# Kernel optimization log

Hardware: AMD Instinct MI355X
Metric: run time of the kernel (lower is better)

Reference implementation:

```python
import jax, jax.numpy as jnp
import numpy as np

N = 102400      # total nodes (2048 molecules x 50 atoms)
E = 409600      # directed edges (avg degree 4)
B = 2048        # number of graphs in batch
F0 = 78         # num_features_mol
OUT = 200       # output_dim
MAXN = 64       # max_num nodes per graph (padding)


def _glorot(key, fan_in, fan_out):
    lim = jnp.sqrt(6.0 / (fan_in + fan_out)).astype(jnp.float32)
    return jax.random.uniform(key, (fan_in, fan_out), jnp.float32, -lim, lim)


def setup_inputs() -> dict:
    key = jax.random.key(0)
    ks = jax.random.split(key, 8)
    x = jax.random.normal(ks[0], (N, F0), jnp.float32)
    edge_index = jax.random.randint(ks[1], (2, E), 0, N, jnp.int32)
    # sorted contiguous graph assignment, 50 nodes per graph
    batch = jnp.repeat(jnp.arange(B, dtype=jnp.int32), N // B)
    return {
        "x": x,
        "edge_index": edge_index,
        "batch": batch,
        "max_num": MAXN,
        "W1": _glorot(ks[2], F0, F0),        "b1": jnp.zeros((F0,), jnp.float32),
        "W2": _glorot(ks[3], F0, 2 * F0),    "b2": jnp.zeros((2 * F0,), jnp.float32),
        "W3": _glorot(ks[4], 2 * F0, 4 * F0),"b3": jnp.zeros((4 * F0,), jnp.float32),
        "Wfc": _glorot(ks[5], 4 * F0, OUT),  "bfc": jnp.zeros((OUT,), jnp.float32),
    }


def _gcn_conv(h, W, b, src, dst, dinv):
    """PyG GCNConv: x' = D^{-1/2}(A+I)D^{-1/2} (x W) + b (with self-loops)."""
    h = h @ W                                  # [N, Fout]
    coef = (dinv[src] * dinv[dst])[:, None]    # [E, 1] symmetric norm
    agg = jax.ops.segment_sum(h[src] * coef, dst, num_segments=N)
    agg = agg + h * (dinv * dinv)[:, None]     # self-loop contribution (norm = 1/deg)
    return agg + b


def reference(x, edge_index, batch, max_num, W1, b1, W2, b2, W3, b3, Wfc, bfc):
    src, dst = edge_index[0], edge_index[1]
    # degree incl. self-loop, computed on destination nodes (PyG gcn_norm)
    deg = jax.ops.segment_sum(jnp.ones((E,), x.dtype), dst, num_segments=N) + 1.0
    dinv = jax.lax.rsqrt(deg)

    h = jax.nn.relu(_gcn_conv(x, W1, b1, src, dst, dinv))
    h = jax.nn.relu(_gcn_conv(h, W2, b2, src, dst, dinv))
    h = jax.nn.relu(_gcn_conv(h, W3, b3, src, dst, dinv))
    h = h @ Wfc + bfc                          # [N, OUT]

    # to_dense_batch: scatter each node into [B, max_num, OUT], truncating
    # nodes beyond max_num per graph (PyG semantics).
    counts = jax.ops.segment_sum(jnp.ones((N,), jnp.int32), batch, num_segments=B)
    starts = jnp.concatenate([jnp.zeros((1,), jnp.int32), jnp.cumsum(counts)[:-1]])
    pos = jnp.arange(N, dtype=jnp.int32) - starts[batch]   # index within graph
    valid = pos < max_num
    flat = jnp.where(valid, batch * max_num + pos, B * max_num)  # dropped -> dummy slot
    dense = jnp.zeros((B * max_num + 1, h.shape[1]), h.dtype).at[flat].set(h)
    return dense[:-1].reshape(B, max_num, h.shape[1])
```

## Files before the change

### kernel.cpp

```cpp
#include <hip/hip_runtime.h>
#include <hip/hip_bf16.h>
#include <stdint.h>

#define N_NODES 102400
#define N_EDGES 409600
#define N_GRAPHS 2048
#define MAXN 64

typedef __attribute__((ext_vector_type(8))) short short8;
typedef __attribute__((ext_vector_type(4))) float f32x4;

static __device__ __forceinline__ float bfu2f(unsigned short u) {
    union { unsigned int i; float f; } v;
    v.i = ((unsigned int)u) << 16;
    return v.f;
}
static __device__ __forceinline__ unsigned short f2bfu(float f) {
    __hip_bfloat16 h = __float2bfloat16(f);
    return *reinterpret_cast<unsigned short*>(&h);
}


__global__ void deg_kernel(const int* __restrict__ dst, int* __restrict__ deg) {
    int e = blockIdx.x * blockDim.x + threadIdx.x;
    if (e < N_EDGES) atomicAdd(&deg[dst[e]], 1);
}

__global__ void scan1_kernel(const int* __restrict__ deg, int* __restrict__ excl,
                             int* __restrict__ bsum) {
    __shared__ int sh[1024];
    int tid = threadIdx.x;
    int gid = blockIdx.x * 1024 + tid;
    int v = deg[gid];
    sh[tid] = v;
    __syncthreads();
    for (int off = 1; off < 1024; off <<= 1) {
        int t = (tid >= off) ? sh[tid - off] : 0;
        __syncthreads();
        sh[tid] += t;
        __syncthreads();
    }
    excl[gid] = sh[tid] - v;
    if (tid == 1023) bsum[blockIdx.x] = sh[tid];
}

__global__ void scan2_kernel(int* __restrict__ bsum) {
    __shared__ int sh[128];
    int tid = threadIdx.x;
    int v = (tid < 100) ? bsum[tid] : 0;
    sh[tid] = v;
    __syncthreads();
    for (int off = 1; off < 128; off <<= 1) {
        int t = (tid >= off) ? sh[tid - off] : 0;
        __syncthreads();
        sh[tid] += t;
        __syncthreads();
    }
    if (tid < 100) bsum[tid] = sh[tid] - v;
}

__global__ void scan3_kernel(const int* __restrict__ excl, const int* __restrict__ bsum,
                             const int* __restrict__ deg,
                             int* __restrict__ offs, int* __restrict__ cursor,
                             float* __restrict__ dinv) {
    int gid = blockIdx.x * blockDim.x + threadIdx.x;
    if (gid < N_NODES) {
        int o = excl[gid] + bsum[gid >> 10];
        offs[gid] = o;
        cursor[gid] = o;
        dinv[gid] = rsqrtf((float)deg[gid] + 1.0f);
    }
    if (gid == 0) offs[N_NODES] = N_EDGES;
}

__global__ void fill_kernel(const int* __restrict__ src, const int* __restrict__ dst,
                            int* __restrict__ cursor, int2* __restrict__ csr_pk,
                            const float* __restrict__ dinv) {
    int e = blockIdx.x * blockDim.x + threadIdx.x;
    if (e >= N_EDGES) return;
    int s = src[e], d = dst[e];
    int pos = atomicAdd(&cursor[d], 1);
    float w = dinv[s] * dinv[d];
    int2 pk;
    pk.x = s;
    pk.y = __float_as_int(w);
    csr_pk[pos] = pk;
}


__global__ void start_kernel(const int* __restrict__ batch, int* __restrict__ startb) {
    int i = blockIdx.x * blockDim.x + threadIdx.x;
    if (i >= N_NODES) return;
    if (i == 0 || batch[i] != batch[i - 1]) startb[batch[i]] = i;
    if (i == 0) startb[N_GRAPHS] = N_NODES;
}

__global__ void rowmap_kernel(const int* __restrict__ batch, const int* __restrict__ startb,
                              const int* __restrict__ pmax, int* __restrict__ rowmap) {
    int i = blockIdx.x * blockDim.x + threadIdx.x;
    if (i >= N_NODES) return;
    int b = batch[i];
    int mx = *pmax;
    int pos = i - startb[b];
    rowmap[i] = (pos < mx) ? (b * mx + pos) : -1;
}

__global__ void padzero_kernel(const int* __restrict__ startb, float* __restrict__ out) {
    int b = blockIdx.x;
    int count = startb[b + 1] - startb[b];
    if (count >= MAXN) return;
    int nel = (MAXN - count) * 100;
    float* base = out + ((size_t)b * MAXN + count) * 200;
    for (int i = threadIdx.x; i < nel; i += 256) {
        float2 z = {0.0f, 0.0f};
        *(float2*)(base + i * 2) = z;
    }
}


__global__ __launch_bounds__(256) void cast_x_kernel(const float* __restrict__ X,
                                                     __hip_bfloat16* __restrict__ xb) {
    int idx = blockIdx.x * blockDim.x + threadIdx.x;
    if (idx >= N_NODES * 48) return;
    int node = idx / 48;
    int c = idx - node * 48;
    int col = c * 2;
    float2 v = {0.0f, 0.0f};
    if (col < 78) v = *(const float2*)(X + (size_t)node * 78 + col);
    __hip_bfloat162 r;
    r.x = __float2bfloat16(v.x);
    r.y = __float2bfloat16(v.y);
    *(__hip_bfloat162*)(xb + (size_t)node * 96 + col) = r;
}


static __device__ __forceinline__ void prep_one(int i, const float* __restrict__ W,
                                                const float* __restrict__ b,
                                                int K, int Nc, int Kp, int Na,
                                                __hip_bfloat16* __restrict__ WT,
                                                float* __restrict__ bp) {
    int total = Na * Kp;
    if (i < total) {
        int c = i / Kp, k = i - c * Kp;
        float v = (c < Nc && k < K) ? W[k * Nc + c] : 0.0f;
        WT[i] = __float2bfloat16(v);
    }
    if (i < Na) bp[i] = (i < Nc) ? b[i] : 0.0f;
}

__global__ void prep_all_kernel(
    const float* __restrict__ W1, const float* __restrict__ b1,
    const float* __restrict__ W2, const float* __restrict__ b2,
    const float* __restrict__ W3, const float* __restrict__ b3,
    const float* __restrict__ Wf, const float* __restrict__ bf,
    __hip_bfloat16* __restrict__ WT1, float* __restrict__ b1p,
    __hip_bfloat16* __restrict__ WT2, float* __restrict__ b2p,
    __hip_bfloat16* __restrict__ WT3, float* __restrict__ b3p,
    __hip_bfloat16* __restrict__ WTF, float* __restrict__ bFp) {
    int i = blockIdx.x * blockDim.x + threadIdx.x;
    if (i < 12288) prep_one(i, W1, b1, 78, 78, 96, 128, WT1, b1p);
    else if (i < 36864) prep_one(i - 12288, W2, b2, 78, 156, 96, 256, WT2, b2p);
    else if (i < 98304) prep_one(i - 36864, W3, b3, 156, 312, 160, 384, WT3, b3p);
    else if (i < 180224) prep_one(i - 98304, Wf, bf, 312, 200, 320, 256, WTF, bFp);
}


template <int LD>
__global__ __launch_bounds__(256) void agg_bf16_v4(
    const __hip_bfloat16* __restrict__ H,
    const int* __restrict__ offs, const int2* __restrict__ csr_pk,
    const float* __restrict__ dinv,
    __hip_bfloat16* __restrict__ out) {
    constexpr int C = LD / 8;
    int idx = blockIdx.x * blockDim.x + threadIdx.x;
    if (idx >= N_NODES * C) return;
    int node = idx / C;
    int c = idx - node * C;
    const unsigned short* Hu = (const unsigned short*)H;
    size_t rowoff = (size_t)node * LD + c * 8;
    float di = dinv[node];
    float sw = di * di;
    short8 h = *(const short8*)(Hu + rowoff);
    float a[8];
#pragma unroll
    for (int i = 0; i < 8; ++i) a[i] = sw * bfu2f((unsigned short)h[i]);
    int e0 = offs[node], e1 = offs[node + 1];
    int j = e0;
    for (; j + 4 <= e1; j += 4) {
        int2 p0 = csr_pk[j], p1 = csr_pk[j + 1], p2 = csr_pk[j + 2], p3 = csr_pk[j + 3];
        float w0 = __int_as_float(p0.y), w1 = __int_as_float(p1.y);
        float w2 = __int_as_float(p2.y), w3 = __int_as_float(p3.y);
        short8 v0 = *(const short8*)(Hu + (size_t)p0.x * LD + c * 8);
        short8 v1 = *(const short8*)(Hu + (size_t)p1.x * LD + c * 8);
        short8 v2 = *(const short8*)(Hu + (size_t)p2.x * LD + c * 8);
        short8 v3 = *(const short8*)(Hu + (size_t)p3.x * LD + c * 8);
#pragma unroll
        for (int i = 0; i < 8; ++i)
            a[i] += w0 * bfu2f((unsigned short)v0[i]) + w1 * bfu2f((unsigned short)v1[i]) +
                    w2 * bfu2f((unsigned short)v2[i]) + w3 * bfu2f((unsigned short)v3[i]);
    }
    for (; j < e1; ++j) {
        int2 pk = csr_pk[j];
        float w = __int_as_float(pk.y);
        short8 v = *(const short8*)(Hu + (size_t)pk.x * LD + c * 8);
#pragma unroll
        for (int i = 0; i < 8; ++i) a[i] += w * bfu2f((unsigned short)v[i]);
    }
    short8 r;
#pragma unroll
    for (int i = 0; i < 8; ++i) r[i] = (short)f2bfu(a[i]);
    *(short8*)((unsigned short*)out + rowoff) = r;
}


template <int FOUT>
__global__ __launch_bounds__(256) void agg_gemm_kernel(
    const __hip_bfloat16* __restrict__ H,
    const int* __restrict__ offs, const int2* __restrict__ csr_pk,
    const float* __restrict__ dinv,
    const __hip_bfloat16* __restrict__ WT,
    const float* __restrict__ biasp,
    __hip_bfloat16* __restrict__ OutH) {
    constexpr int LDH = 96;
    constexpr int NB = FOUT / 32;
    constexpr int STRIDE = 208;
    __shared__ __align__(16) char aggT[128 * STRIDE];
    const int tid = threadIdx.x;
    const int r0 = blockIdx.x * 128;

    {
        const int row = tid >> 1;
        const int cb = (tid & 1) * 6;
        const int node = r0 + row;
        const unsigned short* Hu = (const unsigned short*)H;
        const unsigned short* selfp = Hu + (size_t)node * LDH + cb * 8;
        float di = dinv[node];
        float sw = di * di;
        float a[6][8];
        {
            short8 s[6];
#pragma unroll
            for (int q = 0; q < 6; ++q) s[q] = *(const short8*)(selfp + q * 8);
#pragma unroll
            for (int q = 0; q < 6; ++q)
#pragma unroll
                for (int i = 0; i < 8; ++i) a[q][i] = sw * bfu2f((unsigned short)s[q][i]);
        }
        int e0 = offs[node], e1 = offs[node + 1];
        int j = e0;
        for (; j + 2 <= e1; j += 2) {
            int2 p0 = csr_pk[j], p1 = csr_pk[j + 1];
            float w0 = __int_as_float(p0.y), w1 = __int_as_float(p1.y);
            const unsigned short* q0 = Hu + (size_t)p0.x * LDH + cb * 8;
            const unsigned short* q1 = Hu + (size_t)p1.x * LDH + cb * 8;
            short8 v0[6], v1[6];
#pragma unroll
            for (int q = 0; q < 6; ++q) v0[q] = *(const short8*)(q0 + q * 8);
#pragma unroll
            for (int q = 0; q < 6; ++q) v1[q] = *(const short8*)(q1 + q * 8);
#pragma unroll
            for (int q = 0; q < 6; ++q)
#pragma unroll
                for (int i = 0; i < 8; ++i)
                    a[q][i] += w0 * bfu2f((unsigned short)v0[q][i]) +
                               w1 * bfu2f((unsigned short)v1[q][i]);
        }
        for (; j < e1; ++j) {
            int2 pk = csr_pk[j];
            float w = __int_as_float(pk.y);
            const unsigned short* qp = Hu + (size_t)pk.x * LDH + cb * 8;
            short8 v[6];
#pragma unroll
            for (int q = 0; q < 6; ++q) v[q] = *(const short8*)(qp + q * 8);
#pragma unroll
            for (int q = 0; q < 6; ++q)
#pragma unroll
                for (int i = 0; i < 8; ++i) a[q][i] += w * bfu2f((unsigned short)v[q][i]);
        }
        char* dstrow = aggT + row * STRIDE + cb * 16;
#pragma unroll
        for (int q = 0; q < 6; ++q) {
            short8 r;
#pragma unroll
            for (int i = 0; i < 8; ++i) r[i] = (short)f2bfu(a[q][i]);
            *(short8*)(dstrow + q * 16) = r;
        }
    }
    __syncthreads();

    {
        const int lane = tid & 63;
        const int wid = tid >> 6;
        const int wr = wid >> 1, wc = wid & 1;
        const int frow = lane & 15;
        const int kq = lane >> 4;
        const __hip_bfloat16* bb[NB];
#pragma unroll
        for (int n = 0; n < NB; ++n)
            bb[n] = WT + (size_t)(wc * (FOUT / 2) + n * 16 + frow) * LDH + kq * 8;
        int abase[4];
#pragma unroll
        for (int m = 0; m < 4; ++m)
            abase[m] = (wr * 64 + m * 16 + frow) * STRIDE + kq * 16;

        f32x4 acc[4][NB];
#pragma unroll
        for (int m = 0; m < 4; ++m)
#pragma unroll
            for (int n = 0; n < NB; ++n) {
                f32x4 z = {0.0f, 0.0f, 0.0f, 0.0f};
                acc[m][n] = z;
            }
#pragma unroll
        for (int t = 0; t < 3; ++t) {
            short8 af[4], bfr[NB];
#pragma unroll
            for (int m = 0; m < 4; ++m) af[m] = *(const short8*)(aggT + abase[m] + t * 64);
#pragma unroll
            for (int n = 0; n < NB; ++n) bfr[n] = *(const short8*)(bb[n] + t * 32);
#pragma unroll
            for (int m = 0; m < 4; ++m)
#pragma unroll
                for (int n = 0; n < NB; ++n)
                    acc[m][n] = __builtin_amdgcn_mfma_f32_16x16x32_bf16(bfr[n], af[m],
                                                                        acc[m][n], 0, 0, 0);
        }
#pragma unroll
        for (int m = 0; m < 4; ++m) {
            int row = r0 + wr * 64 + m * 16 + frow;
#pragma unroll
            for (int n = 0; n < NB; ++n) {
                int col0 = wc * (FOUT / 2) + n * 16 + (kq << 2);
                float4 bv = *(const float4*)(biasp + col0);
                ushort4 o;
                o.x = f2bfu(fmaxf(acc[m][n][0] + bv.x, 0.0f));
                o.y = f2bfu(fmaxf(acc[m][n][1] + bv.y, 0.0f));
                o.z = f2bfu(fmaxf(acc[m][n][2] + bv.z, 0.0f));
                o.w = f2bfu(fmaxf(acc[m][n][3] + bv.w, 0.0f));
                *(ushort4*)((unsigned short*)OutH + (size_t)row * FOUT + col0) = o;
            }
        }
    }
}


__global__ __launch_bounds__(256) void gemm3fc_kernel(
    const __hip_bfloat16* __restrict__ A,
    const __hip_bfloat16* __restrict__ W3T,
    const float* __restrict__ b3p,
    const __hip_bfloat16* __restrict__ WTF,
    const float* __restrict__ bFp,
    float* __restrict__ out,
    const int* __restrict__ rowmap) {
    __shared__ __align__(16) char h3[64 * 640];
    const int tid = threadIdx.x;
    const int lane = tid & 63;
    const int w = tid >> 6;
    const int r0 = blockIdx.x * 64;
    const int frow = lane & 15;
    const int kq = lane >> 4;

    {
        const __hip_bfloat16* ab[4];
        const __hip_bfloat16* bb[5];
#pragma unroll
        for (int m = 0; m < 4; ++m)
            ab[m] = A + (size_t)(r0 + m * 16 + frow) * 160 + kq * 8;
#pragma unroll
        for (int n = 0; n < 5; ++n)
            bb[n] = W3T + (size_t)(w * 80 + n * 16 + frow) * 160 + kq * 8;

        f32x4 acc[4][5];
#pragma unroll
        for (int m = 0; m < 4; ++m)
#pragma unroll
            for (int n = 0; n < 5; ++n) {
                f32x4 z = {0.0f, 0.0f, 0.0f, 0.0f};
                acc[m][n] = z;
            }
#pragma unroll
        for (int t = 0; t < 5; ++t) {
            short8 af[4], bfr[5];
#pragma unroll
            for (int m = 0; m < 4; ++m) af[m] = *(const short8*)(ab[m] + t * 32);
#pragma unroll
            for (int n = 0; n < 5; ++n) bfr[n] = *(const short8*)(bb[n] + t * 32);
#pragma unroll
            for (int m = 0; m < 4; ++m)
#pragma unroll
                for (int n = 0; n < 5; ++n)
                    acc[m][n] = __builtin_amdgcn_mfma_f32_16x16x32_bf16(bfr[n], af[m],
                                                                        acc[m][n], 0, 0, 0);
        }
#pragma unroll
        for (int m = 0; m < 4; ++m) {
            int row = m * 16 + frow;
            int swz = (row & 7) << 4;
#pragma unroll
            for (int n = 0; n < 5; ++n) {
                int col0 = w * 80 + n * 16 + (kq << 2);
                float4 bv = *(const float4*)(b3p + col0);
                ushort4 o;
                o.x = f2bfu(fmaxf(acc[m][n][0] + bv.x, 0.0f));
                o.y = f2bfu(fmaxf(acc[m][n][1] + bv.y, 0.0f));
                o.z = f2bfu(fmaxf(acc[m][n][2] + bv.z, 0.0f));
                o.w = f2bfu(fmaxf(acc[m][n][3] + bv.w, 0.0f));
                int byte = row * 640 + col0 * 2;
                *(ushort4*)(h3 + (byte ^ swz)) = o;
            }
        }
    }

    const __hip_bfloat16* bb2[4];
#pragma unroll
    for (int n = 0; n < 4; ++n)
        bb2[n] = WTF + (size_t)(w * 64 + n * 16 + frow) * 320 + kq * 8;
    short8 bfr2[2][4];
#pragma unroll
    for (int n = 0; n < 4; ++n) bfr2[0][n] = *(const short8*)(bb2[n]);
#pragma unroll
    for (int n = 0; n < 4; ++n) bfr2[1][n] = *(const short8*)(bb2[n] + 32);

    __syncthreads();

    {
        int drow_[4];
#pragma unroll
        for (int m = 0; m < 4; ++m) drow_[m] = rowmap[r0 + m * 16 + frow];
        float4 bvF[4];
#pragma unroll
        for (int n = 0; n < 4; ++n)
            bvF[n] = *(const float4*)(bFp + (w * 64 + n * 16 + (kq << 2)));

        int abase[4], aswz[4];
#pragma unroll
        for (int m = 0; m < 4; ++m) {
            int row = m * 16 + frow;
            abase[m] = row * 640 + kq * 16;
            aswz[m] = (row & 7) << 4;
        }
        f32x4 acc[4][4];
#pragma unroll
        for (int m = 0; m < 4; ++m)
#pragma unroll
            for (int n = 0; n < 4; ++n) {
                f32x4 z = {0.0f, 0.0f, 0.0f, 0.0f};
                acc[m][n] = z;
            }
#pragma unroll
        for (int t = 0; t < 10; ++t) {
            short8 af[4];
#pragma unroll
            for (int m = 0; m < 4; ++m)
                af[m] = *(const short8*)(h3 + ((abase[m] + t * 64) ^ aswz[m]));
#pragma unroll
            for (int m = 0; m < 4; ++m)
#pragma unroll
                for (int n = 0; n < 4; ++n)
                    acc[m][n] = __builtin_amdgcn_mfma_f32_16x16x32_bf16(bfr2[t & 1][n], af[m],
                                                                        acc[m][n], 0, 0, 0);
            if (t + 2 < 10) {
#pragma unroll
                for (int n = 0; n < 4; ++n)
                    bfr2[t & 1][n] = *(const short8*)(bb2[n] + (t + 2) * 32);
            }
        }
#pragma unroll
        for (int m = 0; m < 4; ++m) {
            int drow = drow_[m];
            if (drow < 0) continue;
#pragma unroll
            for (int n = 0; n < 4; ++n) {
                int col0 = w * 64 + n * 16 + (kq << 2);
                if (col0 >= 200) continue;
                float4 o;
                o.x = acc[m][n][0] + bvF[n].x;
                o.y = acc[m][n][1] + bvF[n].y;
                o.z = acc[m][n][2] + bvF[n].z;
                o.w = acc[m][n][3] + bvF[n].w;
                *(float4*)(out + (size_t)drow * 200 + col0) = o;
            }
        }
    }
}


static inline char* align256(char* p) {
    return (char*)(((uintptr_t)p + 255) & ~(uintptr_t)255);
}

extern "C" void kernel_launch(void* const* d_in, const int* in_sizes, int n_in,
                              void* d_out, int out_size, void* d_ws, size_t ws_size,
                              hipStream_t stream) {
    const int N = N_NODES, E = N_EDGES;
    const float* x = (const float*)d_in[0];
    const int* ei = (const int*)d_in[1];
    const int* src = ei;
    const int* dst = ei + E;
    const int* batch = (const int*)d_in[2];
    const int* pmax = (const int*)d_in[3];
    const float* W1 = (const float*)d_in[4];
    const float* b1 = (const float*)d_in[5];
    const float* W2 = (const float*)d_in[6];
    const float* b2 = (const float*)d_in[7];
    const float* W3 = (const float*)d_in[8];
    const float* b3 = (const float*)d_in[9];
    const float* Wfc = (const float*)d_in[10];
    const float* bfc = (const float*)d_in[11];
    float* out = (float*)d_out;

    char* p = (char*)d_ws;
    float* dinv = (float*)p;          p = align256(p + (size_t)N * 4);
    int* deg = (int*)p;               p = align256(p + (size_t)N * 4);
    int* offs = (int*)p;              p = align256(p + (size_t)(N + 1) * 4);
    int* cursor = (int*)p;            p = align256(p + (size_t)N * 4);
    int* excl = (int*)p;              p = align256(p + (size_t)N * 4);
    int* bsum = (int*)p;              p = align256(p + 128 * 4);
    int2* csr_pk = (int2*)p;          p = align256(p + (size_t)E * 8);
    int* startb = (int*)p;            p = align256(p + (size_t)(N_GRAPHS + 1) * 4);
    int* rowmap = (int*)p;            p = align256(p + (size_t)N * 4);
    __hip_bfloat16* WT1 = (__hip_bfloat16*)p;  p = align256(p + 128 * 96 * 2);
    float* b1p = (float*)p;           p = align256(p + 128 * 4);
    __hip_bfloat16* WT2 = (__hip_bfloat16*)p;  p = align256(p + 256 * 96 * 2);
    float* b2p = (float*)p;           p = align256(p + 256 * 4);
    __hip_bfloat16* WT3 = (__hip_bfloat16*)p;  p = align256(p + 384 * 160 * 2);
    float* b3p = (float*)p;           p = align256(p + 384 * 4);
    __hip_bfloat16* WTF = (__hip_bfloat16*)p;  p = align256(p + 256 * 320 * 2);
    float* bFp = (float*)p;           p = align256(p + 256 * 4);
    __hip_bfloat16* bufAgg = (__hip_bfloat16*)p;  p = align256(p + (size_t)N * 320 * 2);
    __hip_bfloat16* bufH = (__hip_bfloat16*)p;    p = align256(p + (size_t)N * 320 * 2);

    hipMemsetAsync(deg, 0, (size_t)N * 4, stream);
    deg_kernel<<<(E + 255) / 256, 256, 0, stream>>>(dst, deg);
    scan1_kernel<<<100, 1024, 0, stream>>>(deg, excl, bsum);
    scan2_kernel<<<1, 128, 0, stream>>>(bsum);
    scan3_kernel<<<(N + 255) / 256, 256, 0, stream>>>(excl, bsum, deg, offs, cursor, dinv);
    fill_kernel<<<(E + 255) / 256, 256, 0, stream>>>(src, dst, cursor, csr_pk, dinv);

    start_kernel<<<(N + 255) / 256, 256, 0, stream>>>(batch, startb);
    rowmap_kernel<<<(N + 255) / 256, 256, 0, stream>>>(batch, startb, pmax, rowmap);

    prep_all_kernel<<<(180224 + 255) / 256, 256, 0, stream>>>(
        W1, b1, W2, b2, W3, b3, Wfc, bfc, WT1, b1p, WT2, b2p, WT3, b3p, WTF, bFp);
    cast_x_kernel<<<(N * 48 + 255) / 256, 256, 0, stream>>>(x, bufH);

    agg_gemm_kernel<96><<<N / 128, 256, 0, stream>>>(
        bufH, offs, csr_pk, dinv, WT1, b1p, bufAgg);

    agg_gemm_kernel<160><<<N / 128, 256, 0, stream>>>(
        bufAgg, offs, csr_pk, dinv, WT2, b2p, bufH);

    agg_bf16_v4<160><<<(N * 20 + 255) / 256, 256, 0, stream>>>(bufH, offs, csr_pk, dinv, bufAgg);
    padzero_kernel<<<N_GRAPHS, 256, 0, stream>>>(startb, out);
    gemm3fc_kernel<<<N / 32 * 32 / 64, 256, 0, stream>>>(bufAgg, WT3, b3p, WTF, bFp, out, rowmap);
}
```

Before: 257.9 us.

## Fuse layer-3 neighbor aggregation into the GEMM3+FC kernel via LDS staging

Removes the standalone layer-3 aggregation kernel. The fused GEMM3+FC kernel now gathers neighbor rows for its 64-node tile straight into shared memory (4 threads per row, 40 features each) and feeds the MFMA GEMM from LDS. This drops the global write and re-read of the aggregated 160-wide activation and one launch. It also double-buffers the W3 fragments in registers. The cost is more LDS per block, lower occupancy, and fewer threads issuing the irregular gathers (4 per node instead of 20), which may expose gather latency.

```diff
diff --git a/kernel.cpp b/kernel.cpp
--- a/kernel.cpp
+++ b/kernel.cpp
@@ -165,54 +165,6 @@
 }
 
 
-template <int LD>
-__global__ __launch_bounds__(256) void agg_bf16_v4(
-    const __hip_bfloat16* __restrict__ H,
-    const int* __restrict__ offs, const int2* __restrict__ csr_pk,
-    const float* __restrict__ dinv,
-    __hip_bfloat16* __restrict__ out) {
-    constexpr int C = LD / 8;
-    int idx = blockIdx.x * blockDim.x + threadIdx.x;
-    if (idx >= N_NODES * C) return;
-    int node = idx / C;
-    int c = idx - node * C;
-    const unsigned short* Hu = (const unsigned short*)H;
-    size_t rowoff = (size_t)node * LD + c * 8;
-    float di = dinv[node];
-    float sw = di * di;
-    short8 h = *(const short8*)(Hu + rowoff);
-    float a[8];
-#pragma unroll
-    for (int i = 0; i < 8; ++i) a[i] = sw * bfu2f((unsigned short)h[i]);
-    int e0 = offs[node], e1 = offs[node + 1];
-    int j = e0;
-    for (; j + 4 <= e1; j += 4) {
-        int2 p0 = csr_pk[j], p1 = csr_pk[j + 1], p2 = csr_pk[j + 2], p3 = csr_pk[j + 3];
-        float w0 = __int_as_float(p0.y), w1 = __int_as_float(p1.y);
-        float w2 = __int_as_float(p2.y), w3 = __int_as_float(p3.y);
-        short8 v0 = *(const short8*)(Hu + (size_t)p0.x * LD + c * 8);
-        short8 v1 = *(const short8*)(Hu + (size_t)p1.x * LD + c * 8);
-        short8 v2 = *(const short8*)(Hu + (size_t)p2.x * LD + c * 8);
-        short8 v3 = *(const short8*)(Hu + (size_t)p3.x * LD + c * 8);
-#pragma unroll
-        for (int i = 0; i < 8; ++i)
-            a[i] += w0 * bfu2f((unsigned short)v0[i]) + w1 * bfu2f((unsigned short)v1[i]) +
-                    w2 * bfu2f((unsigned short)v2[i]) + w3 * bfu2f((unsigned short)v3[i]);
-    }
-    for (; j < e1; ++j) {
-        int2 pk = csr_pk[j];
-        float w = __int_as_float(pk.y);
-        short8 v = *(const short8*)(Hu + (size_t)pk.x * LD + c * 8);
-#pragma unroll
-        for (int i = 0; i < 8; ++i) a[i] += w * bfu2f((unsigned short)v[i]);
-    }
-    short8 r;
-#pragma unroll
-    for (int i = 0; i < 8; ++i) r[i] = (short)f2bfu(a[i]);
-    *(short8*)((unsigned short*)out + rowoff) = r;
-}
-
-
 template <int FOUT>
 __global__ __launch_bounds__(256) void agg_gemm_kernel(
     const __hip_bfloat16* __restrict__ H,
@@ -344,14 +296,17 @@
 }
 
 
-__global__ __launch_bounds__(256) void gemm3fc_kernel(
-    const __hip_bfloat16* __restrict__ A,
+__global__ __launch_bounds__(256) void agg_gemm3fc_kernel(
+    const __hip_bfloat16* __restrict__ H,
+    const int* __restrict__ offs, const int2* __restrict__ csr_pk,
+    const float* __restrict__ dinv,
     const __hip_bfloat16* __restrict__ W3T,
     const float* __restrict__ b3p,
     const __hip_bfloat16* __restrict__ WTF,
     const float* __restrict__ bFp,
     float* __restrict__ out,
     const int* __restrict__ rowmap) {
+    __shared__ __align__(16) char aggT[64 * 336];
     __shared__ __align__(16) char h3[64 * 640];
     const int tid = threadIdx.x;
     const int lane = tid & 63;
@@ -361,14 +316,80 @@
     const int kq = lane >> 4;
 
     {
-        const __hip_bfloat16* ab[4];
-        const __hip_bfloat16* bb[5];
-#pragma unroll
-        for (int m = 0; m < 4; ++m)
-            ab[m] = A + (size_t)(r0 + m * 16 + frow) * 160 + kq * 8;
-#pragma unroll
-        for (int n = 0; n < 5; ++n)
-            bb[n] = W3T + (size_t)(w * 80 + n * 16 + frow) * 160 + kq * 8;
+        const int row = tid >> 2;
+        const int qb = (tid & 3) * 5;
+        const int node = r0 + row;
+        const unsigned short* Hu = (const unsigned short*)H;
+        const unsigned short* selfp = Hu + (size_t)node * 160 + qb * 8;
+        float di = dinv[node];
+        float sw = di * di;
+        float a[5][8];
+        {
+            short8 s[5];
+#pragma unroll
+            for (int q = 0; q < 5; ++q) s[q] = *(const short8*)(selfp + q * 8);
+#pragma unroll
+            for (int q = 0; q < 5; ++q)
+#pragma unroll
+                for (int i = 0; i < 8; ++i) a[q][i] = sw * bfu2f((unsigned short)s[q][i]);
+        }
+        int e0 = offs[node], e1 = offs[node + 1];
+        int j = e0;
+        for (; j + 2 <= e1; j += 2) {
+            int2 p0 = csr_pk[j], p1 = csr_pk[j + 1];
+            float w0 = __int_as_float(p0.y), w1 = __int_as_float(p1.y);
+            const unsigned short* q0 = Hu + (size_t)p0.x * 160 + qb * 8;
+            const unsigned short* q1 = Hu + (size_t)p1.x * 160 + qb * 8;
+            short8 v0[5], v1[5];
+#pragma unroll
+            for (int q = 0; q < 5; ++q) v0[q] = *(const short8*)(q0 + q * 8);
+#pragma unroll
+            for (int q = 0; q < 5; ++q) v1[q] = *(const short8*)(q1 + q * 8);
+#pragma unroll
+            for (int q = 0; q < 5; ++q)
+#pragma unroll
+                for (int i = 0; i < 8; ++i)
+                    a[q][i] += w0 * bfu2f((unsigned short)v0[q][i]) +
+                               w1 * bfu2f((unsigned short)v1[q][i]);
+        }
+        for (; j < e1; ++j) {
+            int2 pk = csr_pk[j];
+            float ww = __int_as_float(pk.y);
+            const unsigned short* qp = Hu + (size_t)pk.x * 160 + qb * 8;
+            short8 v[5];
+#pragma unroll
+            for (int q = 0; q < 5; ++q) v[q] = *(const short8*)(qp + q * 8);
+#pragma unroll
+            for (int q = 0; q < 5; ++q)
+#pragma unroll
+                for (int i = 0; i < 8; ++i) a[q][i] += ww * bfu2f((unsigned short)v[q][i]);
+        }
+        char* dstrow = aggT + row * 336 + qb * 16;
+#pragma unroll
+        for (int q = 0; q < 5; ++q) {
+            short8 r;
+#pragma unroll
+            for (int i = 0; i < 8; ++i) r[i] = (short)f2bfu(a[q][i]);
+            *(short8*)(dstrow + q * 16) = r;
+        }
+    }
+
+    const __hip_bfloat16* bb1[5];
+#pragma unroll
+    for (int n = 0; n < 5; ++n)
+        bb1[n] = W3T + (size_t)(w * 80 + n * 16 + frow) * 160 + kq * 8;
+    short8 bw[2][5];
+#pragma unroll
+    for (int n = 0; n < 5; ++n) bw[0][n] = *(const short8*)(bb1[n]);
+#pragma unroll
+    for (int n = 0; n < 5; ++n) bw[1][n] = *(const short8*)(bb1[n] + 32);
+
+    __syncthreads();
+
+    {
+        int abase1[4];
+#pragma unroll
+        for (int m = 0; m < 4; ++m) abase1[m] = (m * 16 + frow) * 336 + kq * 16;
 
         f32x4 acc[4][5];
 #pragma unroll
@@ -380,17 +401,20 @@
             }
 #pragma unroll
         for (int t = 0; t < 5; ++t) {
-            short8 af[4], bfr[5];
-#pragma unroll
-            for (int m = 0; m < 4; ++m) af[m] = *(const short8*)(ab[m] + t * 32);
-#pragma unroll
-            for (int n = 0; n < 5; ++n) bfr[n] = *(const short8*)(bb[n] + t * 32);
+            short8 af[4];
+#pragma unroll
+            for (int m = 0; m < 4; ++m) af[m] = *(const short8*)(aggT + abase1[m] + t * 64);
 #pragma unroll
             for (int m = 0; m < 4; ++m)
 #pragma unroll
                 for (int n = 0; n < 5; ++n)
-                    acc[m][n] = __builtin_amdgcn_mfma_f32_16x16x32_bf16(bfr[n], af[m],
+                    acc[m][n] = __builtin_amdgcn_mfma_f32_16x16x32_bf16(bw[t & 1][n], af[m],
                                                                         acc[m][n], 0, 0, 0);
+            if (t + 2 < 5) {
+#pragma unroll
+                for (int n = 0; n < 5; ++n)
+                    bw[t & 1][n] = *(const short8*)(bb1[n] + (t + 2) * 32);
+            }
         }
 #pragma unroll
         for (int m = 0; m < 4; ++m) {
@@ -550,7 +574,7 @@
     agg_gemm_kernel<160><<<N / 128, 256, 0, stream>>>(
         bufAgg, offs, csr_pk, dinv, WT2, b2p, bufH);
 
-    agg_bf16_v4<160><<<(N * 20 + 255) / 256, 256, 0, stream>>>(bufH, offs, csr_pk, dinv, bufAgg);
     padzero_kernel<<<N_GRAPHS, 256, 0, stream>>>(startb, out);
-    gemm3fc_kernel<<<N / 32 * 32 / 64, 256, 0, stream>>>(bufAgg, WT3, b3p, WTF, bFp, out, rowmap);
-}
+    agg_gemm3fc_kernel<<<N / 64, 256, 0, stream>>>(
+        bufH, offs, csr_pk, dinv, WT3, b3p, WTF, bFp, out, rowmap);
+}
```

New measurement: 269.6 us. +4.5%, slower.
